# Performance work log

Measured on AMD Instinct MI355X. Metric: run time of the kernel, lower is better.

The kernel has to match this reference:

```python
import jax, jax.numpy as jnp
import numpy as np

B = 4096
HID = 1024
Z1P = 256
Z1R = 256
Z2P = 128
Z2R = 128
N_STEP = 32


def _gru_cell(x, h, Wih, Whh, bih, bhh):
    # torch.nn.GRUCell math. Wih: [3H, in], Whh: [3H, H]
    gi = x @ Wih.T + bih  # [B, 3H]
    gh = h @ Whh.T + bhh  # [B, 3H]
    i_r, i_z, i_n = jnp.split(gi, 3, axis=1)
    h_r, h_z, h_n = jnp.split(gh, 3, axis=1)
    r = jax.nn.sigmoid(i_r + h_r)
    zg = jax.nn.sigmoid(i_z + h_z)
    n = jnp.tanh(i_n + r * h_n)
    return (1.0 - zg) * n + zg * h


def _decode(z, Wi, bi, Wih, Whh, bih, bhh, Wo, bo, out_dim):
    b = z.shape[0]
    h0 = jnp.tanh(z @ Wi.T + bi)  # linear_init + tanh
    out0 = jnp.zeros((b, out_dim), z.dtype).at[:, -1].set(1.0)  # SOS token

    def step(carry, _):
        out, h = carry
        x = jnp.concatenate([out, z], axis=1)  # [B, out_dim + z_dim]
        h = _gru_cell(x, h, Wih, Whh, bih, bhh)
        o = h @ Wo.T + bo  # linear_out
        return (o, h), o

    _, xs = jax.lax.scan(step, (out0, h0), None, length=N_STEP)  # xs: [T, B, out_dim]
    return jnp.transpose(xs, (1, 0, 2))  # [B, T, out_dim]


def setup_inputs() -> dict:
    key = jax.random.key(0)
    ks = jax.random.split(key, 24)
    s = lambda fan_in: 1.0 / np.sqrt(fan_in)
    u = lambda k, shape, fan_in: jax.random.uniform(k, shape, jnp.float32, -s(fan_in), s(fan_in))
    inp = {
        "z_8p": jax.random.normal(ks[0], (B, Z1P), jnp.float32),
        "z_8r": jax.random.normal(ks[1], (B, Z1R), jnp.float32),
        "z_4p": jax.random.normal(ks[2], (B, Z2P), jnp.float32),
        "z_4r": jax.random.normal(ks[3], (B, Z2R), jnp.float32),
        # linear_init_0 / linear_init_1
        "Wi0": u(ks[4], (HID, Z1P), Z1P), "bi0": u(ks[5], (HID,), Z1P),
        "Wi1": u(ks[6], (HID, Z1R), Z1R), "bi1": u(ks[7], (HID,), Z1R),
        # grucell_0 (input = z1p + z2p)
        "Wih0": u(ks[8], (3 * HID, Z1P + Z2P), HID), "Whh0": u(ks[9], (3 * HID, HID), HID),
        "bih0": u(ks[10], (3 * HID,), HID), "bhh0": u(ks[11], (3 * HID,), HID),
        # grucell_1 (input = z1r + z2r)
        "Wih1": u(ks[12], (3 * HID, Z1R + Z2R), HID), "Whh1": u(ks[13], (3 * HID, HID), HID),
        "bih1": u(ks[14], (3 * HID,), HID), "bhh1": u(ks[15], (3 * HID,), HID),
        # linear_out_0 / linear_out_1
        "Wo0": u(ks[16], (Z2P, HID), HID), "bo0": u(ks[17], (Z2P,), HID),
        "Wo1": u(ks[18], (Z2R, HID), HID), "bo1": u(ks[19], (Z2R,), HID),
    }
    return inp


def reference(z_8p, z_8r, z_4p, z_4r,
              Wi0, bi0, Wi1, bi1,
              Wih0, Whh0, bih0, bhh0,
              Wih1, Whh1, bih1, bhh1,
              Wo0, bo0, Wo1, bo1):
    # eval-mode forward; z_4p / z_4r are only cached during training and do not
    # affect the output (teacher-forcing branches in the source are no-ops).
    z4p = _decode(z_8p, Wi0, bi0, Wih0, Whh0, bih0, bhh0, Wo0, bo0, Z2P)
    z4r = _decode(z_8r, Wi1, bi1, Wih1, Whh1, bih1, bhh1, Wo1, bo1, Z2R)
    return (z4p, z4r)
```

## Files before the change

### kernel.cpp

```cpp
#include <hip/hip_runtime.h>
#include <stdint.h>


typedef unsigned short u16;
typedef __attribute__((ext_vector_type(8))) short bf8v;
typedef __attribute__((ext_vector_type(4))) float f4v;

constexpr int DECN = 2;
constexpr int BB = 4096;
constexpr int HH = 1024;
constexpr int ZZ = 256;
constexpr int OO = 128;
constexpr int TT = 32;
constexpr int GG = 3 * HH;
constexpr int WR = 4 * HH + OO;
constexpr int ILD = OO + ZZ;
constexpr int BK = 64;
constexpr int NKT = HH / BK;

__device__ __forceinline__ float bf2f(u16 u) {
  uint32_t x = ((uint32_t)u) << 16;
  return __builtin_bit_cast(float, x);
}
__device__ __forceinline__ u16 f2bf(float f) {
  uint32_t x = __builtin_bit_cast(uint32_t, f);
  x += 0x7fffu + ((x >> 16) & 1u);
  return (u16)(x >> 16);
}
__device__ __forceinline__ float sigf(float x) { return 1.f / (1.f + __expf(-x)); }
__device__ __forceinline__ float tanh_fast(float x) { return 2.f / (1.f + __expf(-2.f * x)) - 1.f; }

__device__ __forceinline__ void load16(const u16* g, u16* l) {
  __builtin_amdgcn_global_load_lds(
      (const __attribute__((address_space(1))) unsigned int*)g,
      (__attribute__((address_space(3))) unsigned int*)l, 16, 0, 0);
}

template <int NSEC>
__device__ __forceinline__ void gemm_core(
    const u16* __restrict__ A, int lda,
    const u16* __restrict__ Bm, int ldb,
    const int (&brow)[NSEC], int m0, int K,
    u16* Als, u16* Bls, f4v (&acc)[NSEC][4][2]) {
  const int tid = threadIdx.x;
  const int lane = tid & 63;
  const int wid = tid >> 6;
  const int wm = wid >> 1, wn = wid & 1;
  const int srow = lane >> 2;
  const int scol = (lane & 3) * 8;
  const int l15 = lane & 15;
  const int khalf = (lane >> 4) * 8;

  for (int k0 = 0; k0 < K; k0 += 32) {
    const u16* ga = A + (size_t)(m0 + wid * 16 + srow) * lda + k0 + scol;
    load16(ga, Als + (wid * 16) * 32);
    load16(ga + (size_t)64 * lda, Als + (64 + wid * 16) * 32);
#pragma unroll
    for (int s = 0; s < NSEC; ++s) {
      const u16* gb = Bm + (size_t)(brow[s] + wid * 16 + srow) * ldb + k0 + scol;
      load16(gb, Bls + (s * 64 + wid * 16) * 32);
    }
    __syncthreads();
    bf8v af[4];
#pragma unroll
    for (int mf = 0; mf < 4; ++mf)
      af[mf] = *(const bf8v*)(Als + (wm * 64 + mf * 16 + l15) * 32 + khalf);
#pragma unroll
    for (int s = 0; s < NSEC; ++s) {
#pragma unroll
      for (int nf = 0; nf < 2; ++nf) {
        bf8v bv = *(const bf8v*)(Bls + (s * 64 + wn * 32 + nf * 16 + l15) * 32 + khalf);
#pragma unroll
        for (int mf = 0; mf < 4; ++mf)
          acc[s][mf][nf] = __builtin_amdgcn_mfma_f32_16x16x32_bf16(af[mf], bv, acc[s][mf][nf], 0, 0, 0);
      }
    }
    __syncthreads();
  }
}


__global__ __launch_bounds__(256) void pack_kernel(const float* __restrict__ src, int ld, int col0,
                                                   u16* __restrict__ dst, int rows, int cols) {
  int i = blockIdx.x * 256 + threadIdx.x;
  if (i < rows * cols) {
    int r = i / cols, c = i - r * cols;
    dst[i] = f2bf(src[(size_t)r * ld + col0 + c]);
  }
}

__global__ __launch_bounds__(256) void wot_kernel(const float* __restrict__ wo, u16* __restrict__ dst) {
  int i = blockIdx.x * 256 + threadIdx.x;
  if (i < HH * OO) {
    int k = i / OO, c = i - k * OO;
    dst[i] = f2bf(wo[(size_t)c * HH + k]);
  }
}

__global__ __launch_bounds__(256) void vec_kernel(
    const float* __restrict__ wih0, const float* __restrict__ wih1,
    const float* __restrict__ bih0, const float* __restrict__ bih1,
    const float* __restrict__ bhh0, const float* __restrict__ bhh1,
    const float* __restrict__ bo0, const float* __restrict__ bo1,
    float* __restrict__ d1, float* __restrict__ v2) {
  int i = blockIdx.x * 256 + threadIdx.x;
  if (i >= DECN * GG) return;
  int dec = i / GG, j = i - dec * GG;
  const float* wih = dec ? wih1 : wih0;
  const float* bo = dec ? bo1 : bo0;
  const float* bih = dec ? bih1 : bih0;
  const float* bhh = dec ? bhh1 : bhh0;
  float bc = 0.f;
  for (int c = 0; c < OO; ++c) bc += wih[(size_t)j * ILD + c] * bo[c];
  d1[i] = wih[(size_t)j * ILD + (OO - 1)] - bc;
  v2[i] = bih[j] + (j < 2 * HH ? bhh[j] : 0.f) + bc;
}

__global__ __launch_bounds__(256, 2) void comb_kernel(
    const u16* __restrict__ wio, const u16* __restrict__ wot,
    const float* __restrict__ whh0, const float* __restrict__ whh1,
    u16* __restrict__ wb2) {
  __shared__ u16 Als[128 * 32];
  __shared__ u16 Bls[64 * 32];
  const int dec = blockIdx.z, m0 = blockIdx.x * 128, n0 = blockIdx.y * 64;
  const int lane = threadIdx.x & 63, wid = threadIdx.x >> 6;
  const int wm = wid >> 1, wn = wid & 1;
  const int rbase = m0 + wm * 64 + ((lane >> 4) << 2);
  const int clb = wn * 32 + (lane & 15);
  int brow[1] = {n0};
  f4v acc[1][4][2];
#pragma unroll
  for (int mf = 0; mf < 4; ++mf)
#pragma unroll
    for (int nf = 0; nf < 2; ++nf)
#pragma unroll
      for (int r = 0; r < 4; ++r) acc[0][mf][nf][r] = 0.f;
  gemm_core<1>(wio + (size_t)dec * GG * OO, OO, wot + (size_t)dec * HH * OO, OO, brow, m0, OO, Als, Bls, acc);
  const float* whh = dec ? whh1 : whh0;
  u16* W2 = wb2 + (size_t)dec * WR * HH;
#pragma unroll
  for (int mf = 0; mf < 4; ++mf)
#pragma unroll
    for (int nf = 0; nf < 2; ++nf) {
      const int k = n0 + clb + nf * 16;
#pragma unroll
      for (int r = 0; r < 4; ++r) {
        const int j = rbase + mf * 16 + r;
        float v = acc[0][mf][nf][r] + (j < 2 * HH ? whh[(size_t)j * HH + k] : 0.f);
        W2[(size_t)j * HH + k] = f2bf(v);
      }
    }
}

__global__ __launch_bounds__(256, 2) void gzc_kernel(
    const u16* __restrict__ zbf, const u16* __restrict__ wzb,
    const float* __restrict__ v2, u16* __restrict__ gzc) {
  __shared__ u16 Als[128 * 32];
  __shared__ u16 Bls[64 * 32];
  const int dec = blockIdx.z, m0 = blockIdx.x * 128, n0 = blockIdx.y * 64;
  const int lane = threadIdx.x & 63, wid = threadIdx.x >> 6;
  const int wm = wid >> 1, wn = wid & 1;
  const int rbase = m0 + wm * 64 + ((lane >> 4) << 2);
  const int clb = wn * 32 + (lane & 15);
  int brow[1] = {n0};
  f4v acc[1][4][2];
#pragma unroll
  for (int mf = 0; mf < 4; ++mf)
#pragma unroll
    for (int nf = 0; nf < 2; ++nf)
#pragma unroll
      for (int r = 0; r < 4; ++r) acc[0][mf][nf][r] = 0.f;
  gemm_core<1>(zbf + (size_t)dec * BB * ZZ, ZZ, wzb + (size_t)dec * GG * ZZ, ZZ, brow, m0, ZZ, Als, Bls, acc);
  const float* vv = v2 + dec * GG;
  u16* out = gzc + (size_t)dec * BB * GG;
#pragma unroll
  for (int mf = 0; mf < 4; ++mf)
#pragma unroll
    for (int nf = 0; nf < 2; ++nf) {
      const int col = n0 + clb + nf * 16;
#pragma unroll
      for (int r = 0; r < 4; ++r) {
        const int row = rbase + mf * 16 + r;
        out[(size_t)row * GG + col] = f2bf(acc[0][mf][nf][r] + vv[col]);
      }
    }
}

__global__ __launch_bounds__(256, 2) void h0_kernel(
    const u16* __restrict__ zbf, const u16* __restrict__ wib,
    const float* __restrict__ bi0, const float* __restrict__ bi1,
    float* __restrict__ hf, u16* __restrict__ hbf) {
  __shared__ u16 Als[128 * 32];
  __shared__ u16 Bls[64 * 32];
  const int dec = blockIdx.z, m0 = blockIdx.x * 128, n0 = blockIdx.y * 64;
  const int lane = threadIdx.x & 63, wid = threadIdx.x >> 6;
  const int wm = wid >> 1, wn = wid & 1;
  const int rbase = m0 + wm * 64 + ((lane >> 4) << 2);
  const int clb = wn * 32 + (lane & 15);
  int brow[1] = {n0};
  f4v acc[1][4][2];
#pragma unroll
  for (int mf = 0; mf < 4; ++mf)
#pragma unroll
    for (int nf = 0; nf < 2; ++nf)
#pragma unroll
      for (int r = 0; r < 4; ++r) acc[0][mf][nf][r] = 0.f;
  gemm_core<1>(zbf + (size_t)dec * BB * ZZ, ZZ, wib + (size_t)dec * HH * ZZ, ZZ, brow, m0, ZZ, Als, Bls, acc);
  const float* bi = dec ? bi1 : bi0;
  float* ho = hf + (size_t)dec * 2 * BB * HH;
  u16* hb = hbf + (size_t)dec * 2 * BB * HH;
#pragma unroll
  for (int mf = 0; mf < 4; ++mf)
#pragma unroll
    for (int nf = 0; nf < 2; ++nf) {
      const int col = n0 + clb + nf * 16;
#pragma unroll
      for (int r = 0; r < 4; ++r) {
        const int row = rbase + mf * 16 + r;
        float v = tanh_fast(acc[0][mf][nf][r] + bi[col]);
        ho[(size_t)row * HH + col] = v;
        hb[(size_t)row * HH + col] = f2bf(v);
      }
    }
}

template <int NS>
__device__ __forceinline__ void kloop8(
    const u16* __restrict__ A, const u16* __restrict__ W,
    const int (&brow)[4], int m0, u16* lds, int lane, int wid,
    f4v (&acc)[8][4]) {
  const int wm = wid >> 2, wn = wid & 3;
  const int l15 = lane & 15, lq = lane >> 4;
  const int srow = wid * 8 + (lane >> 3);
  const int sgc = (lane & 7) ^ ((lane >> 3) & 7);

  auto stA = [&](int kt, int r) {
    const u16* g = A + (size_t)(m0 + r * 64 + srow) * HH + kt * BK + sgc * 8;
    load16(g, lds + ((kt & 1) * 2) * 16384 + (r * 64 + wid * 8) * 64);
  };
  auto stB = [&](int kt, int r) {
    const u16* g = W + (size_t)(brow[r] + srow) * HH + kt * BK + sgc * 8;
    load16(g, lds + ((kt & 1) * 2 + 1) * 16384 + (r * 64 + wid * 8) * 64);
  };

  stB(0, 0); stB(0, 1); stB(0, 2); stB(0, 3);
  stA(0, 0); stA(0, 1); stA(0, 2); stA(0, 3);
  asm volatile("s_waitcnt vmcnt(0)" ::: "memory");
  __builtin_amdgcn_s_barrier();

  auto tile = [&](int kt, bool pf) {
    const u16* la = lds + (size_t)(kt & 1) * 32768;
    const u16* lb = la + 16384;
    bf8v bfr[NS][2];
#pragma unroll
    for (int q = 0; q < 4; ++q) {
      if (q == 0) {
#pragma unroll
        for (int s = 0; s < NS; ++s)
#pragma unroll
          for (int ks = 0; ks < 2; ++ks)
            bfr[s][ks] = *(const bf8v*)&lb[(s * 64 + wn * 16 + l15) * 64 +
                                           (((ks * 4 + lq) ^ (l15 & 7)) * 8)];
      }
      bf8v aq[2][2];
#pragma unroll
      for (int mi = 0; mi < 2; ++mi)
#pragma unroll
        for (int ks = 0; ks < 2; ++ks)
          aq[mi][ks] = *(const bf8v*)&la[(wm * 128 + (2 * q + mi) * 16 + l15) * 64 +
                                         (((ks * 4 + lq) ^ (l15 & 7)) * 8)];
      if (pf) {
        if (q == 0) { stB(kt + 1, 0); stB(kt + 1, 1); }
        if (q == 1) { stB(kt + 1, 2); stB(kt + 1, 3); }
        if (q == 2) { stA(kt + 1, 0); stA(kt + 1, 2); }
        if (q == 3) { stA(kt + 1, 1); stA(kt + 1, 3); }
      }
      __builtin_amdgcn_s_barrier();
      asm volatile("s_waitcnt lgkmcnt(0)" ::: "memory");
      __builtin_amdgcn_s_setprio(1);
#pragma unroll
      for (int mi = 0; mi < 2; ++mi)
#pragma unroll
        for (int s = 0; s < NS; ++s)
#pragma unroll
          for (int ks = 0; ks < 2; ++ks)
            acc[2 * q + mi][s] = __builtin_amdgcn_mfma_f32_16x16x32_bf16(
                aq[mi][ks], bfr[s][ks], acc[2 * q + mi][s], 0, 0, 0);
      __builtin_amdgcn_s_setprio(0);
      if (q == 1) {
        if (pf) asm volatile("s_waitcnt vmcnt(4)" ::: "memory");
        else    asm volatile("s_waitcnt vmcnt(0)" ::: "memory");
      }
      if (q == 3) {
        asm volatile("s_waitcnt vmcnt(2)" ::: "memory");
      }
      __builtin_amdgcn_s_barrier();
    }
  };
  for (int kt = 0; kt < NKT - 1; ++kt) tile(kt, true);
  tile(NKT - 1, false);
}

__global__ __launch_bounds__(512, 2) void step8_kernel(
    const u16* __restrict__ hbf_in, const float* __restrict__ hf_in,
    float* __restrict__ hf_out, u16* __restrict__ hbf_out,
    const u16* __restrict__ Wb, const u16* __restrict__ gzc,
    const float* __restrict__ d1,
    const float* __restrict__ bhh0v, const float* __restrict__ bhh1v,
    const float* __restrict__ bo0v, const float* __restrict__ bo1v,
    float* __restrict__ dout, int step1, int o_slot, int y_base) {
  __shared__ u16 lds[4 * 16384];
  const int dec = blockIdx.z;
  const int ntile = blockIdx.y + y_base;
  const int m0 = blockIdx.x * 256;
  const int lane = threadIdx.x & 63, wid = threadIdx.x >> 6;
  const int wm = wid >> 2, wn = wid & 3;
  const int l15 = lane & 15, lq = lane >> 4;
  const u16* A = hbf_in + (size_t)dec * 2 * BB * HH;
  const u16* W = Wb + (size_t)dec * WR * HH;

  f4v acc[8][4];
#pragma unroll
  for (int mf = 0; mf < 8; ++mf)
#pragma unroll
    for (int s = 0; s < 4; ++s)
#pragma unroll
      for (int r = 0; r < 4; ++r) acc[mf][s][r] = 0.f;

  if (ntile < 16) {
    const int j0 = ntile * 64;
    int brow[4] = {j0, HH + j0, 2 * HH + j0, 3 * HH + j0};
    kloop8<4>(A, W, brow, m0, lds, lane, wid, acc);

    const u16* gz = gzc + (size_t)dec * BB * GG;
    const float* dd = d1 + dec * GG;
    const float* bhhn = (dec ? bhh1v : bhh0v) + 2 * HH;
    const float* hold = hf_in + (size_t)dec * 2 * BB * HH;
    float* hnew = hf_out + (size_t)dec * 2 * BB * HH;
    u16* hnb = hbf_out + (size_t)dec * 2 * BB * HH;
    const int col = j0 + wn * 16 + l15;
    const float bn = bhhn[col];
    const float dr0 = step1 ? dd[col] : 0.f;
    const float dr1 = step1 ? dd[HH + col] : 0.f;
    const float dr2 = step1 ? dd[2 * HH + col] : 0.f;
#pragma unroll
    for (int mf = 0; mf < 8; ++mf) {
#pragma unroll
      for (int r = 0; r < 4; ++r) {
        const int row = m0 + wm * 128 + mf * 16 + lq * 4 + r;
        const size_t ro = (size_t)row * GG;
        float v0 = acc[mf][0][r] + bf2f(gz[ro + col]) + dr0;
        float v1 = acc[mf][1][r] + bf2f(gz[ro + HH + col]) + dr1;
        float v2 = acc[mf][2][r] + bf2f(gz[ro + 2 * HH + col]) + dr2;
        float v3 = acc[mf][3][r] + bn;
        float rg = sigf(v0), zg = sigf(v1);
        float nn = tanh_fast(v2 + rg * v3);
        float hv = hold[(size_t)row * HH + col];
        float hn = (1.f - zg) * nn + zg * hv;
        hnew[(size_t)row * HH + col] = hn;
        hnb[(size_t)row * HH + col] = f2bf(hn);
      }
    }
  } else {
    int brow[4] = {4 * HH, 4 * HH + 64, 4 * HH, 4 * HH + 64};
    kloop8<2>(A, W, brow, m0, lds, lane, wid, acc);
    const float* bod = dec ? bo1v : bo0v;
    float* op = dout + (size_t)dec * BB * TT * OO + (size_t)o_slot * OO;
#pragma unroll
    for (int mf = 0; mf < 8; ++mf)
#pragma unroll
      for (int s2 = 0; s2 < 2; ++s2) {
        const int col = s2 * 64 + wn * 16 + l15;
        const float b = bod[col];
#pragma unroll
        for (int r = 0; r < 4; ++r) {
          const int row = m0 + wm * 128 + mf * 16 + lq * 4 + r;
          op[(size_t)row * TT * OO + col] = acc[mf][s2][r] + b;
        }
      }
  }
}


extern "C" void kernel_launch(void* const* d_in, const int* in_sizes, int n_in,
                              void* d_out, int out_size, void* d_ws, size_t ws_size,
                              hipStream_t stream) {
  const float* z8[2] = {(const float*)d_in[0], (const float*)d_in[1]};
  const float* Wi[2] = {(const float*)d_in[4], (const float*)d_in[6]};
  const float* bi[2] = {(const float*)d_in[5], (const float*)d_in[7]};
  const float* Wih[2] = {(const float*)d_in[8], (const float*)d_in[12]};
  const float* Whh[2] = {(const float*)d_in[9], (const float*)d_in[13]};
  const float* bih[2] = {(const float*)d_in[10], (const float*)d_in[14]};
  const float* bhh[2] = {(const float*)d_in[11], (const float*)d_in[15]};
  const float* Wo[2] = {(const float*)d_in[16], (const float*)d_in[18]};
  const float* bo[2] = {(const float*)d_in[17], (const float*)d_in[19]};
  float* dout = (float*)d_out;

  char* p = (char*)d_ws;
  size_t off = 0;
  auto carve = [&](size_t nbytes) {
    char* r = p + off;
    off += (nbytes + 255) & ~(size_t)255;
    return (void*)r;
  };
  float* hf = (float*)carve((size_t)DECN * 2 * BB * HH * 4);
  u16* hbf = (u16*)carve((size_t)DECN * 2 * BB * HH * 2);
  u16* gzc = (u16*)carve((size_t)DECN * BB * GG * 2);
  u16* wb1 = (u16*)carve((size_t)DECN * WR * HH * 2);
  u16* wb2 = (u16*)carve((size_t)DECN * WR * HH * 2);
  u16* zbf = (u16*)carve((size_t)DECN * BB * ZZ * 2);
  u16* wzb = (u16*)carve((size_t)DECN * GG * ZZ * 2);
  u16* wio = (u16*)carve((size_t)DECN * GG * OO * 2);
  u16* wib = (u16*)carve((size_t)DECN * HH * ZZ * 2);
  u16* wot = (u16*)carve((size_t)DECN * HH * OO * 2);
  float* d1v = (float*)carve((size_t)DECN * GG * 4);
  float* v2v = (float*)carve((size_t)DECN * GG * 4);
  (void)ws_size; (void)in_sizes; (void)n_in; (void)out_size;

  auto pack = [&](const float* src, int ld, int c0, u16* dst, int rows, int cols) {
    int n = rows * cols;
    pack_kernel<<<(n + 255) / 256, 256, 0, stream>>>(src, ld, c0, dst, rows, cols);
  };
  for (int d = 0; d < 2; ++d) {
    pack(z8[d], ZZ, 0, zbf + (size_t)d * BB * ZZ, BB, ZZ);
    pack(Wih[d], ILD, OO, wzb + (size_t)d * GG * ZZ, GG, ZZ);
    pack(Wih[d], ILD, 0, wio + (size_t)d * GG * OO, GG, OO);
    pack(Wi[d], ZZ, 0, wib + (size_t)d * HH * ZZ, HH, ZZ);
    pack(Whh[d], HH, 0, wb1 + (size_t)d * WR * HH, 2 * HH, HH);
    pack(Whh[d] + (size_t)2 * HH * HH, HH, 0, wb1 + (size_t)d * WR * HH + (size_t)3 * HH * HH, HH, HH);
    pack(Whh[d] + (size_t)2 * HH * HH, HH, 0, wb2 + (size_t)d * WR * HH + (size_t)3 * HH * HH, HH, HH);
    pack(Wo[d], HH, 0, wb2 + (size_t)d * WR * HH + (size_t)4 * HH * HH, OO, HH);
    wot_kernel<<<(HH * OO + 255) / 256, 256, 0, stream>>>(Wo[d], wot + (size_t)d * HH * OO);
    hipMemsetAsync(wb1 + (size_t)d * WR * HH + (size_t)2 * HH * HH, 0, (size_t)HH * HH * 2, stream);
  }
  vec_kernel<<<(DECN * GG + 255) / 256, 256, 0, stream>>>(
      Wih[0], Wih[1], bih[0], bih[1], bhh[0], bhh[1], bo[0], bo[1], d1v, v2v);
  comb_kernel<<<dim3(24, 16, 2), 256, 0, stream>>>(wio, wot, Whh[0], Whh[1], wb2);
  gzc_kernel<<<dim3(32, 48, 2), 256, 0, stream>>>(zbf, wzb, v2v, gzc);
  h0_kernel<<<dim3(32, 16, 2), 256, 0, stream>>>(zbf, wib, bi[0], bi[1], hf, hbf);

  for (int t = 1; t <= TT; ++t) {
    const int bin = (t - 1) & 1, bout = t & 1;
    dim3 grid(16, t == 1 ? 16 : 17, 2);
    step8_kernel<<<grid, 512, 0, stream>>>(
        hbf + (size_t)bin * BB * HH, hf + (size_t)bin * BB * HH,
        hf + (size_t)bout * BB * HH, hbf + (size_t)bout * BB * HH,
        t == 1 ? wb1 : wb2, gzc, d1v, bhh[0], bhh[1], bo[0], bo[1],
        dout, t == 1 ? 1 : 0, t - 2, 0);
  }
  step8_kernel<<<dim3(16, 1, 2), 512, 0, stream>>>(
      hbf, hf, hf + (size_t)BB * HH, hbf + (size_t)BB * HH,
      wb2, gzc, d1v, bhh[0], bhh[1], bo[0], bo[1],
      dout, 0, TT - 1, 16);
}
```

Before: 3.209 ms.

## Transpose gate/hidden buffers and batch output projection after recurrence

```diff
diff --git a/kernel.cpp b/kernel.cpp
--- a/kernel.cpp
+++ b/kernel.cpp
@@ -5,6 +5,7 @@
 typedef unsigned short u16;
 typedef __attribute__((ext_vector_type(8))) short bf8v;
 typedef __attribute__((ext_vector_type(4))) float f4v;
+typedef __attribute__((ext_vector_type(4))) unsigned short us4v;
 
 constexpr int DECN = 2;
 constexpr int BB = 4096;
@@ -154,7 +155,7 @@
 
 __global__ __launch_bounds__(256, 2) void gzc_kernel(
     const u16* __restrict__ zbf, const u16* __restrict__ wzb,
-    const float* __restrict__ v2, u16* __restrict__ gzc) {
+    const float* __restrict__ v2, u16* __restrict__ gzt) {
   __shared__ u16 Als[128 * 32];
   __shared__ u16 Bls[64 * 32];
   const int dec = blockIdx.z, m0 = blockIdx.x * 128, n0 = blockIdx.y * 64;
@@ -172,24 +173,24 @@
       for (int r = 0; r < 4; ++r) acc[0][mf][nf][r] = 0.f;
   gemm_core<1>(zbf + (size_t)dec * BB * ZZ, ZZ, wzb + (size_t)dec * GG * ZZ, ZZ, brow, m0, ZZ, Als, Bls, acc);
   const float* vv = v2 + dec * GG;
-  u16* out = gzc + (size_t)dec * BB * GG;
+  u16* out = gzt + (size_t)dec * 3 * HH * BB;
 #pragma unroll
   for (int mf = 0; mf < 4; ++mf)
 #pragma unroll
     for (int nf = 0; nf < 2; ++nf) {
-      const int col = n0 + clb + nf * 16;
-#pragma unroll
-      for (int r = 0; r < 4; ++r) {
-        const int row = rbase + mf * 16 + r;
-        out[(size_t)row * GG + col] = f2bf(acc[0][mf][nf][r] + vv[col]);
-      }
+      const int colg = n0 + clb + nf * 16;
+      const int g = colg >> 10, cc = colg & 1023;
+      us4v v;
+#pragma unroll
+      for (int r = 0; r < 4; ++r) v[r] = f2bf(acc[0][mf][nf][r] + vv[colg]);
+      *(us4v*)(out + ((size_t)g * HH + cc) * BB + rbase + mf * 16) = v;
     }
 }
 
 __global__ __launch_bounds__(256, 2) void h0_kernel(
     const u16* __restrict__ zbf, const u16* __restrict__ wib,
     const float* __restrict__ bi0, const float* __restrict__ bi1,
-    float* __restrict__ hf, u16* __restrict__ hbf) {
+    float* __restrict__ hft, u16* __restrict__ hst, int slots) {
   __shared__ u16 Als[128 * 32];
   __shared__ u16 Bls[64 * 32];
   const int dec = blockIdx.z, m0 = blockIdx.x * 128, n0 = blockIdx.y * 64;
@@ -207,20 +208,22 @@
       for (int r = 0; r < 4; ++r) acc[0][mf][nf][r] = 0.f;
   gemm_core<1>(zbf + (size_t)dec * BB * ZZ, ZZ, wib + (size_t)dec * HH * ZZ, ZZ, brow, m0, ZZ, Als, Bls, acc);
   const float* bi = dec ? bi1 : bi0;
-  float* ho = hf + (size_t)dec * 2 * BB * HH;
-  u16* hb = hbf + (size_t)dec * 2 * BB * HH;
+  float* ho = hft + (size_t)dec * 2 * HH * BB;
+  u16* hb = hst + (size_t)dec * slots * BB * HH;
 #pragma unroll
   for (int mf = 0; mf < 4; ++mf)
 #pragma unroll
     for (int nf = 0; nf < 2; ++nf) {
       const int col = n0 + clb + nf * 16;
+      f4v hv;
 #pragma unroll
       for (int r = 0; r < 4; ++r) {
         const int row = rbase + mf * 16 + r;
         float v = tanh_fast(acc[0][mf][nf][r] + bi[col]);
-        ho[(size_t)row * HH + col] = v;
+        hv[r] = v;
         hb[(size_t)row * HH + col] = f2bf(v);
       }
+      *(f4v*)(ho + (size_t)col * BB + rbase + mf * 16) = hv;
     }
 }
 
@@ -302,13 +305,13 @@
 }
 
 __global__ __launch_bounds__(512, 2) void step8_kernel(
-    const u16* __restrict__ hbf_in, const float* __restrict__ hf_in,
-    float* __restrict__ hf_out, u16* __restrict__ hbf_out,
-    const u16* __restrict__ Wb, const u16* __restrict__ gzc,
+    const u16* __restrict__ hst, float* __restrict__ hft,
+    const u16* __restrict__ Wb, const u16* __restrict__ gzt,
     const float* __restrict__ d1,
     const float* __restrict__ bhh0v, const float* __restrict__ bhh1v,
     const float* __restrict__ bo0v, const float* __restrict__ bo1v,
-    float* __restrict__ dout, int step1, int o_slot, int y_base) {
+    float* __restrict__ dout, int step1, int o_slot, int y_base,
+    int slots, int slot_in, int slot_out, int sin, int sout) {
   __shared__ u16 lds[4 * 16384];
   const int dec = blockIdx.z;
   const int ntile = blockIdx.y + y_base;
@@ -316,7 +319,8 @@
   const int lane = threadIdx.x & 63, wid = threadIdx.x >> 6;
   const int wm = wid >> 2, wn = wid & 3;
   const int l15 = lane & 15, lq = lane >> 4;
-  const u16* A = hbf_in + (size_t)dec * 2 * BB * HH;
+  const size_t SZ = (size_t)BB * HH;
+  const u16* A = hst + ((size_t)dec * slots + slot_in) * SZ;
   const u16* W = Wb + (size_t)dec * WR * HH;
 
   f4v acc[8][4];
@@ -332,34 +336,40 @@
     int brow[4] = {j0, HH + j0, 2 * HH + j0, 3 * HH + j0};
     kloop8<4>(A, W, brow, m0, lds, lane, wid, acc);
 
-    const u16* gz = gzc + (size_t)dec * BB * GG;
+    const int col = j0 + wn * 16 + l15;
     const float* dd = d1 + dec * GG;
-    const float* bhhn = (dec ? bhh1v : bhh0v) + 2 * HH;
-    const float* hold = hf_in + (size_t)dec * 2 * BB * HH;
-    float* hnew = hf_out + (size_t)dec * 2 * BB * HH;
-    u16* hnb = hbf_out + (size_t)dec * 2 * BB * HH;
-    const int col = j0 + wn * 16 + l15;
-    const float bn = bhhn[col];
+    const float bn = ((dec ? bhh1v : bhh0v) + 2 * HH)[col];
     const float dr0 = step1 ? dd[col] : 0.f;
     const float dr1 = step1 ? dd[HH + col] : 0.f;
     const float dr2 = step1 ? dd[2 * HH + col] : 0.f;
+    const u16* gzb = gzt + (size_t)dec * 3 * HH * BB;
+    const u16* g0p = gzb + (size_t)col * BB;
+    const u16* g1p = gzb + ((size_t)HH + col) * BB;
+    const u16* g2p = gzb + ((size_t)2 * HH + col) * BB;
+    const float* hvp = hft + ((size_t)dec * 2 + sin) * ((size_t)HH * BB) + (size_t)col * BB;
+    float* hop = hft + ((size_t)dec * 2 + sout) * ((size_t)HH * BB) + (size_t)col * BB;
+    u16* hnbp = (u16*)hst + ((size_t)dec * slots + slot_out) * SZ;
 #pragma unroll
     for (int mf = 0; mf < 8; ++mf) {
+      const int row0 = m0 + wm * 128 + mf * 16 + lq * 4;
+      us4v g0 = *(const us4v*)(g0p + row0);
+      us4v g1 = *(const us4v*)(g1p + row0);
+      us4v g2 = *(const us4v*)(g2p + row0);
+      f4v hv4 = *(const f4v*)(hvp + row0);
+      f4v hn4;
 #pragma unroll
       for (int r = 0; r < 4; ++r) {
-        const int row = m0 + wm * 128 + mf * 16 + lq * 4 + r;
-        const size_t ro = (size_t)row * GG;
-        float v0 = acc[mf][0][r] + bf2f(gz[ro + col]) + dr0;
-        float v1 = acc[mf][1][r] + bf2f(gz[ro + HH + col]) + dr1;
-        float v2 = acc[mf][2][r] + bf2f(gz[ro + 2 * HH + col]) + dr2;
+        float v0 = acc[mf][0][r] + bf2f(g0[r]) + dr0;
+        float v1 = acc[mf][1][r] + bf2f(g1[r]) + dr1;
+        float v2 = acc[mf][2][r] + bf2f(g2[r]) + dr2;
         float v3 = acc[mf][3][r] + bn;
         float rg = sigf(v0), zg = sigf(v1);
         float nn = tanh_fast(v2 + rg * v3);
-        float hv = hold[(size_t)row * HH + col];
-        float hn = (1.f - zg) * nn + zg * hv;
-        hnew[(size_t)row * HH + col] = hn;
-        hnb[(size_t)row * HH + col] = f2bf(hn);
-      }
+        float hn = (1.f - zg) * nn + zg * hv4[r];
+        hn4[r] = hn;
+        hnbp[(size_t)(row0 + r) * HH + col] = f2bf(hn);
+      }
+      *(f4v*)(hop + row0) = hn4;
     }
   } else {
     int brow[4] = {4 * HH, 4 * HH + 64, 4 * HH, 4 * HH + 64};
@@ -379,6 +389,47 @@
         }
       }
   }
+}
+
+__global__ __launch_bounds__(512, 2) void ogemm_kernel(
+    const u16* __restrict__ hst, const u16* __restrict__ Wb,
+    const float* __restrict__ bo0v, const float* __restrict__ bo1v,
+    float* __restrict__ dout) {
+  __shared__ u16 lds[4 * 16384];
+  const int dec = blockIdx.z;
+  const int m0 = blockIdx.x * 256;
+  const int lane = threadIdx.x & 63, wid = threadIdx.x >> 6;
+  const int wm = wid >> 2, wn = wid & 3;
+  const int l15 = lane & 15, lq = lane >> 4;
+  const size_t SZ = (size_t)BB * HH;
+  const u16* A = hst + (size_t)dec * 33 * SZ + SZ;
+  const u16* W = Wb + (size_t)dec * WR * HH;
+
+  f4v acc[8][4];
+#pragma unroll
+  for (int mf = 0; mf < 8; ++mf)
+#pragma unroll
+    for (int s = 0; s < 4; ++s)
+#pragma unroll
+      for (int r = 0; r < 4; ++r) acc[mf][s][r] = 0.f;
+
+  int brow[4] = {4 * HH, 4 * HH + 64, 4 * HH, 4 * HH + 64};
+  kloop8<2>(A, W, brow, m0, lds, lane, wid, acc);
+  const float* bod = dec ? bo1v : bo0v;
+  float* op = dout + (size_t)dec * BB * TT * OO;
+#pragma unroll
+  for (int mf = 0; mf < 8; ++mf)
+#pragma unroll
+    for (int s2 = 0; s2 < 2; ++s2) {
+      const int col = s2 * 64 + wn * 16 + l15;
+      const float b = bod[col];
+#pragma unroll
+      for (int r = 0; r < 4; ++r) {
+        const int mrow = m0 + wm * 128 + mf * 16 + lq * 4 + r;
+        const int t = mrow >> 12, bb = mrow & (BB - 1);
+        op[(size_t)bb * TT * OO + t * OO + col] = acc[mf][s2][r] + b;
+      }
+    }
 }
 
 
@@ -396,6 +447,10 @@
   const float* bo[2] = {(const float*)d_in[17], (const float*)d_in[19]};
   float* dout = (float*)d_out;
 
+  const size_t SZ = (size_t)BB * HH;
+  const bool big = ws_size >= (size_t)760 * 1024 * 1024;
+  const int slots = big ? 33 : 2;
+
   char* p = (char*)d_ws;
   size_t off = 0;
   auto carve = [&](size_t nbytes) {
@@ -403,9 +458,9 @@
     off += (nbytes + 255) & ~(size_t)255;
     return (void*)r;
   };
-  float* hf = (float*)carve((size_t)DECN * 2 * BB * HH * 4);
-  u16* hbf = (u16*)carve((size_t)DECN * 2 * BB * HH * 2);
-  u16* gzc = (u16*)carve((size_t)DECN * BB * GG * 2);
+  float* hft = (float*)carve((size_t)DECN * 2 * SZ * 4);
+  u16* hst = (u16*)carve((size_t)DECN * slots * SZ * 2);
+  u16* gzt = (u16*)carve((size_t)DECN * 3 * HH * BB * 2);
   u16* wb1 = (u16*)carve((size_t)DECN * WR * HH * 2);
   u16* wb2 = (u16*)carve((size_t)DECN * WR * HH * 2);
   u16* zbf = (u16*)carve((size_t)DECN * BB * ZZ * 2);
@@ -415,7 +470,7 @@
   u16* wot = (u16*)carve((size_t)DECN * HH * OO * 2);
   float* d1v = (float*)carve((size_t)DECN * GG * 4);
   float* v2v = (float*)carve((size_t)DECN * GG * 4);
-  (void)ws_size; (void)in_sizes; (void)n_in; (void)out_size;
+  (void)in_sizes; (void)n_in; (void)out_size;
 
   auto pack = [&](const float* src, int ld, int c0, u16* dst, int rows, int cols) {
     int n = rows * cols;
@@ -436,20 +491,23 @@
   vec_kernel<<<(DECN * GG + 255) / 256, 256, 0, stream>>>(
       Wih[0], Wih[1], bih[0], bih[1], bhh[0], bhh[1], bo[0], bo[1], d1v, v2v);
   comb_kernel<<<dim3(24, 16, 2), 256, 0, stream>>>(wio, wot, Whh[0], Whh[1], wb2);
-  gzc_kernel<<<dim3(32, 48, 2), 256, 0, stream>>>(zbf, wzb, v2v, gzc);
-  h0_kernel<<<dim3(32, 16, 2), 256, 0, stream>>>(zbf, wib, bi[0], bi[1], hf, hbf);
+  gzc_kernel<<<dim3(32, 48, 2), 256, 0, stream>>>(zbf, wzb, v2v, gzt);
+  h0_kernel<<<dim3(32, 16, 2), 256, 0, stream>>>(zbf, wib, bi[0], bi[1], hft, hst, slots);
 
   for (int t = 1; t <= TT; ++t) {
-    const int bin = (t - 1) & 1, bout = t & 1;
-    dim3 grid(16, t == 1 ? 16 : 17, 2);
+    const int slot_in = big ? t - 1 : (t - 1) & 1;
+    const int slot_out = big ? t : t & 1;
+    const int sin = (t - 1) & 1, sout = t & 1;
+    dim3 grid(16, big ? 16 : (t == 1 ? 16 : 17), 2);
     step8_kernel<<<grid, 512, 0, stream>>>(
-        hbf + (size_t)bin * BB * HH, hf + (size_t)bin * BB * HH,
-        hf + (size_t)bout * BB * HH, hbf + (size_t)bout * BB * HH,
-        t == 1 ? wb1 : wb2, gzc, d1v, bhh[0], bhh[1], bo[0], bo[1],
-        dout, t == 1 ? 1 : 0, t - 2, 0);
-  }
-  step8_kernel<<<dim3(16, 1, 2), 512, 0, stream>>>(
-      hbf, hf, hf + (size_t)BB * HH, hbf + (size_t)BB * HH,
-      wb2, gzc, d1v, bhh[0], bhh[1], bo[0], bo[1],
-      dout, 0, TT - 1, 16);
-}
+        hst, hft, t == 1 ? wb1 : wb2, gzt, d1v, bhh[0], bhh[1], bo[0], bo[1],
+        dout, t == 1 ? 1 : 0, t - 2, 0, slots, slot_in, slot_out, sin, sout);
+  }
+  if (big) {
+    ogemm_kernel<<<dim3(512, 1, 2), 512, 0, stream>>>(hst, wb2, bo[0], bo[1], dout);
+  } else {
+    step8_kernel<<<dim3(16, 1, 2), 512, 0, stream>>>(
+        hst, hft, wb2, gzt, d1v, bhh[0], bhh[1], bo[0], bo[1],
+        dout, 0, TT - 1, 16, slots, 0, 1, 0, 1);
+  }
+}
```

New measurement: 3.131 ms. -2.4%, faster.
